# Optimization experiments

Hardware: AMD Instinct MI355X
Metric: run time of the kernel (lower is better)

The kernel has to match this reference:

```python
import jax, jax.numpy as jnp
import numpy as np

BATCH, SEQ, D_DIM, H = 8, 4096, 256, 64


def _log_step_init(u, dmin=0.001, dmax=0.1):
    lg_dmin, lg_dmax = np.log(dmin), np.log(dmax)
    return u * (lg_dmax - lg_dmin) + lg_dmin


def _make_hippo_nplr(N):
    q = np.arange(N)
    hip = np.sqrt((2 * q[:, None] + 1) * (2 * q[None, :] + 1))
    hip = np.where(q[:, None] > q[None, :], hip, 0.0) + np.diag(q + 1.0)
    hip = -hip
    p = np.sqrt(q + 0.5)
    S = hip + np.outer(p, p)  # NPLR: A = S - p p^T
    lam, V = np.linalg.eig(S)
    P = V.conj().T @ p
    B = V.conj().T @ (np.sqrt(2.0) * p)
    return lam.astype(np.complex64), P.astype(np.complex64), B.astype(np.complex64)


def _ri(z):
    return np.stack([z.real, z.imag], axis=-1).astype(np.float32)


def _cx(p):
    return p[..., 0] + 1j * p[..., 1]


def setup_inputs() -> dict:
    key = jax.random.key(0)
    k1, k2, k3 = jax.random.split(key, 3)
    lam, P, B = _make_hippo_nplr(H)
    lam_ri = jnp.asarray(_ri(lam))                      # (H, 2)
    P_ri = jnp.asarray(_ri(P))                          # (H, 2)
    B_ri = jnp.asarray(np.tile(_ri(B)[None], (D_DIM, 1, 1)))  # (D, H, 2)
    C_ri = jax.random.uniform(k1, (D_DIM, H, 2), dtype=jnp.float32)  # torch.rand complex
    Dp = jnp.ones((1, 1, D_DIM), dtype=jnp.float32)
    log_delta = jnp.asarray(
        _log_step_init(np.asarray(jax.random.uniform(k2, (D_DIM,), dtype=jnp.float32)))
    ).astype(jnp.float32)
    x = jax.random.normal(k3, (BATCH, SEQ, D_DIM), dtype=jnp.float32)
    return {"x": x, "lam_ri": lam_ri, "P_ri": P_ri, "B_ri": B_ri,
            "C_ri": C_ri, "D": Dp, "log_delta": log_delta}


def reference(x, lam_ri, P_ri, B_ri, C_ri, D, log_delta):
    # S4 DPLR generating-function kernel via Woodbury / Cauchy dot-products + iFFT conv.
    lam, P, B, C = _cx(lam_ri), _cx(P_ri), _cx(B_ri), _cx(C_ri)  # (H,), (H,), (D,H), (D,H)
    delta = jnp.exp(log_delta)                                   # (D,)
    L = x.shape[1]
    z = jnp.exp(2j * jnp.pi * jnp.arange(L) / L).astype(jnp.complex64)  # roots of unity (L,)
    coef = 2.0 / (1.0 + z)                                        # (L,)
    g = (2.0 * (1.0 - z) / (1.0 + z))[None, :] / delta[:, None].astype(jnp.complex64)  # (D, L)
    cauchy = 1.0 / (g[:, :, None] - lam[None, None, :])           # (D, L, H) -- R(z) diagonal
    # Woodbury: C (R - R P P* R / (1 + P* R P)) B  as 4 Cauchy dot products
    k00 = jnp.einsum("dh,dlh->dl", C * B, cauchy)
    k01 = jnp.einsum("dh,dlh->dl", C * P[None, :], cauchy)
    k10 = jnp.einsum("dh,dlh->dl", P.conj()[None, :] * B, cauchy)
    k11 = jnp.einsum("h,dlh->dl", P.conj() * P, cauchy)
    at_roots = coef[None, :] * (k00 - k01 * k10 / (1.0 + k11))    # (D, L)
    K = jnp.fft.ifft(at_roots, axis=-1).real.astype(x.dtype)      # (D, L) time-domain kernel
    # circular convolution along the sequence axis, per channel
    Xf = jnp.fft.fft(x, axis=1)                                   # (B, L, D)
    Kf = jnp.fft.fft(K, axis=-1)                                  # (D, L)
    y = jnp.fft.ifft(Xf * Kf.T[None, :, :], axis=1).real.astype(x.dtype)
    return y + D * x
```

## Files before the change

kernel.cpp:

```cpp
#include <hip/hip_runtime.h>
#include <math.h>

#ifndef M_PI
#define M_PI 3.14159265358979323846
#endif

#define BB 8
#define LL 4096
#define DD 256
#define HH 64

__device__ __forceinline__ float2 cmulf(float2 a, float2 b) {
    return make_float2(a.x*b.x - a.y*b.y, a.x*b.y + a.y*b.x);
}
__device__ __forceinline__ float2 cmul_cs(float2 a, float c, float s) {
    return make_float2(a.x*c - a.y*s, a.x*s + a.y*c);
}
__device__ __forceinline__ float2 cadd(float2 a, float2 b){return make_float2(a.x+b.x, a.y+b.y);}
__device__ __forceinline__ float2 csub(float2 a, float2 b){return make_float2(a.x-b.x, a.y-b.y);}

#define DR4(i) ((((i)&3)<<2)|((i)>>2))
#define SPW(k) ((((k)>>4)*17) + ((k)&15))

template<int SGN>
__device__ __forceinline__ void r4(float2& a, float2& b, float2& c, float2& d) {
    float2 e0 = cadd(a, c), e1 = csub(a, c);
    float2 o0 = cadd(b, d), o1 = csub(b, d);
    float2 j1 = (SGN < 0) ? make_float2(o1.y, -o1.x) : make_float2(-o1.y, o1.x);
    a = cadd(e0, o0);
    b = cadd(e1, j1);
    c = csub(e0, o0);
    d = csub(e1, j1);
}

template<int SGN>
__device__ __forceinline__ void fft16(float2 v[16]) {
    const float C16[10] = {1.f, 0.92387953f, 0.70710678f, 0.38268343f, 0.f,
                           -0.38268343f, -0.70710678f, -0.92387953f, -1.f, -0.92387953f};
    const float S16[10] = {0.f, 0.38268343f, 0.70710678f, 0.92387953f, 1.f,
                           0.92387953f, 0.70710678f, 0.38268343f, 0.f, -0.38268343f};
#pragma unroll
    for (int a0 = 0; a0 < 4; ++a0)
        r4<SGN>(v[a0], v[a0+4], v[a0+8], v[a0+12]);
#pragma unroll
    for (int a0 = 1; a0 < 4; ++a0) {
#pragma unroll
        for (int j0 = 1; j0 < 4; ++j0) {
            const int e = a0*j0;
            const float cc = C16[e];
            const float ss = (SGN < 0) ? -S16[e] : S16[e];
            v[a0 + 4*j0] = cmul_cs(v[a0 + 4*j0], cc, ss);
        }
    }
#pragma unroll
    for (int j0 = 0; j0 < 4; ++j0)
        r4<SGN>(v[4*j0+0], v[4*j0+1], v[4*j0+2], v[4*j0+3]);
}

__device__ __forceinline__ float2 woodbury_coef(
    float k00r, float k00i, float k01r, float k01i,
    float k10r, float k10i, float k11r, float k11i, float tc)
{
    float wr = 1.f + k11r, wi = k11i;
    float winv = __builtin_amdgcn_rcpf(wr*wr + wi*wi);
    float qr = k01r*k10r - k01i*k10i;
    float qi = k01r*k10i + k01i*k10r;
    float dr = (qr*wr + qi*wi) * winv;
    float di = (qi*wr - qr*wi) * winv;
    float rr = k00r - dr, ri = k00i - di;
    return make_float2(rr - tc*ri, tc*rr + ri);
}

__global__ __launch_bounds__(256)
void s4_cauchy_kf(const float* __restrict__ lam_ri,
                  const float* __restrict__ P_ri,
                  const float* __restrict__ B_ri,
                  const float* __restrict__ C_ri,
                  const float* __restrict__ Dp,
                  const float* __restrict__ log_delta,
                  float2* __restrict__ Kf)
{
    __shared__ float4 WA[HH];
    __shared__ float4 WB[HH];
    __shared__ float  WC[HH];
    const int d   = blockIdx.y;
    const int tid = threadIdx.x;
    if (tid < HH) {
        const int h = tid;
        float br = B_ri[(d*HH + h)*2 + 0], bi = B_ri[(d*HH + h)*2 + 1];
        float cr = C_ri[(d*HH + h)*2 + 0], ci = C_ri[(d*HH + h)*2 + 1];
        float pr = P_ri[h*2 + 0], pi = P_ri[h*2 + 1];
        WA[h] = make_float4(cr*br - ci*bi, cr*bi + ci*br,
                            cr*pr - ci*pi, cr*pi + ci*pr);
        WB[h] = make_float4(pr*br + pi*bi, pr*bi - pi*br,
                            pr*pr + pi*pi, -lam_ri[h*2+0]);
        WC[h] = lam_ri[h*2+1];
    }
    __syncthreads();
    const int l = blockIdx.x * blockDim.x + tid;
    if (l > 2048) return;
    const float delta = expf(log_delta[d]);
    const float dterm = Dp[d];
    const float SCALE = 0.5f / 4096.f;

    if (l == 2048) {
        float sr = 0.f;
        for (int h = 0; h < HH; ++h) sr += WA[h].x;
        Kf[(size_t)d*LL + 2048] = make_float2((0.5f*delta*sr + dterm)*SCALE, 0.f);
        return;
    }

    float sn, cs;
    sincosf((float)l * (float)(M_PI/4096.0), &sn, &cs);
    const float t = sn * __builtin_amdgcn_rcpf(cs);
    const float G = -2.f * t * __builtin_amdgcn_rcpf(delta);

    float a00r=0,a00i=0,a01r=0,a01i=0,a10r=0,a10i=0,a11r=0,a11i=0;
    float b00r=0,b00i=0,b01r=0,b01i=0,b10r=0,b10i=0,b11r=0,b11i=0;

#pragma unroll 4
    for (int h = 0; h < HH; ++h) {
        const float4 wa = WA[h];
        const float4 wb = WB[h];
        const float  lih = WC[h];
        const float  nr  = wb.w;
        const float  nr2 = nr*nr;
        {
            const float ni  = G - lih;
            const float inv = __builtin_amdgcn_rcpf(nr2 + ni*ni);
            const float rr  = nr*inv, ri = -ni*inv;
            a00r += wa.x*rr - wa.y*ri;  a00i += wa.x*ri + wa.y*rr;
            a01r += wa.z*rr - wa.w*ri;  a01i += wa.z*ri + wa.w*rr;
            a10r += wb.x*rr - wb.y*ri;  a10i += wb.x*ri + wb.y*rr;
            a11r += wb.z*rr;            a11i += wb.z*ri;
        }
        {
            const float ni  = -G - lih;
            const float inv = __builtin_amdgcn_rcpf(nr2 + ni*ni);
            const float rr  = nr*inv, ri = -ni*inv;
            b00r += wa.x*rr - wa.y*ri;  b00i += wa.x*ri + wa.y*rr;
            b01r += wa.z*rr - wa.w*ri;  b01i += wa.z*ri + wa.w*rr;
            b10r += wb.x*rr - wb.y*ri;  b10i += wb.x*ri + wb.y*rr;
            b11r += wb.z*rr;            b11i += wb.z*ri;
        }
    }

    float2 ar1 = woodbury_coef(a00r,a00i,a01r,a01i,a10r,a10i,a11r,a11i, -t);
    float2 ar2 = woodbury_coef(b00r,b00i,b01r,b01i,b10r,b10i,b11r,b11i, +t);

    float2 kf = make_float2((0.5f*(ar1.x + ar2.x) + dterm)*SCALE,
                            (0.5f*(ar1.y - ar2.y))*SCALE);
    Kf[(size_t)d*LL + l] = kf;
}

__global__ __launch_bounds__(256)
void s4_fftconv(const float* __restrict__ x, const float2* __restrict__ Kf,
                float* __restrict__ y)
{
    __shared__ float2 As[4352];
    const int tid = threadIdx.x;
    const int p  = ((blockIdx.x & 7) << 7) | (blockIdx.x >> 3);
    const int b  = p >> 7;
    const int d2 = p & 127;

    const float2* xp = (const float2*)x + ((size_t)b*LL)*(DD/2) + d2;
    float2*       yp = (float2*)y       + ((size_t)b*LL)*(DD/2) + d2;

    float2 v[16];

    {
        const int r = tid;
#pragma unroll
        for (int a = 0; a < 16; ++a)
            v[a] = xp[(size_t)(a*256 + r)*(DD/2)];
        fft16<-1>(v);
        float2 base; sincosf(-(float)(2.0*M_PI/4096.0)*(float)r, &base.y, &base.x);
        float2 w = make_float2(1.f, 0.f);
#pragma unroll
        for (int k0 = 0; k0 < 16; ++k0) {
            As[17*r + k0] = cmulf(v[DR4(k0)], w);
            w = cmulf(w, base);
        }
    }
    __syncthreads();

    {
        const int k0 = tid >> 4, c = tid & 15;
#pragma unroll
        for (int bb = 0; bb < 16; ++bb)
            v[bb] = As[272*bb + 17*c + k0];
        __syncthreads();
        fft16<-1>(v);
        float2 base; sincosf(-(float)(2.0*M_PI/256.0)*(float)c, &base.y, &base.x);
        float2 w = make_float2(1.f, 0.f);
#pragma unroll
        for (int m0 = 0; m0 < 16; ++m0) {
            As[272*k0 + 17*c + m0] = cmulf(v[DR4(m0)], w);
            w = cmulf(w, base);
        }
    }
    __syncthreads();

    {
        const int k0 = tid >> 4, m0 = tid & 15;
#pragma unroll
        for (int c = 0; c < 16; ++c)
            v[c] = As[272*k0 + 17*c + m0];
        __syncthreads();
        fft16<-1>(v);
        const int s17 = 17*m0 + k0;
#pragma unroll
        for (int m1 = 0; m1 < 16; ++m1)
            As[s17 + 272*m1] = v[DR4(m1)];
    }
    __syncthreads();

    {
        const float2* Keb = Kf + (size_t)(2*d2)  *LL;
        const float2* Kob = Kf + (size_t)(2*d2+1)*LL;
#pragma unroll
        for (int i = 0; i < 9; ++i) {
            int k = tid + (i << 8);
            if (k <= 2048) {
                int mk = (4096 - k) & 4095;
                float2 Zk = As[SPW(k)];
                float2 Zm = As[SPW(mk)];
                float2 Ke = Keb[k];
                float2 Ko = Kob[k];
                float2 S  = make_float2(Ke.x + Ko.x, Ke.y + Ko.y);
                float2 Df = make_float2(Ke.x - Ko.x, Ke.y - Ko.y);
                float2 cZm = make_float2(Zm.x, -Zm.y);
                float2 t0 = cmulf(Zk,  S);
                float2 t1 = cmulf(cZm, Df);
                float2 t2 = cmulf(cZm, S);
                float2 t3 = cmulf(Zk,  Df);
                As[SPW(k)]  = make_float2(t0.x + t1.x,   t0.y + t1.y);
                As[SPW(mk)] = make_float2(t2.x + t3.x, -(t2.y + t3.y));
            }
        }
    }
    __syncthreads();

    {
        const int k0 = tid >> 4, m0 = tid & 15;
        const int s17 = 17*m0 + k0;
#pragma unroll
        for (int m1 = 0; m1 < 16; ++m1)
            v[m1] = As[s17 + 272*m1];
        __syncthreads();
        fft16<1>(v);
        float2 base; sincosf((float)(2.0*M_PI/256.0)*(float)m0, &base.y, &base.x);
        float2 w = make_float2(1.f, 0.f);
#pragma unroll
        for (int c = 0; c < 16; ++c) {
            As[272*k0 + 17*c + m0] = cmulf(v[DR4(c)], w);
            w = cmulf(w, base);
        }
    }
    __syncthreads();

    {
        const int k0 = tid >> 4, c = tid & 15;
#pragma unroll
        for (int m0 = 0; m0 < 16; ++m0)
            v[m0] = As[272*k0 + 17*c + m0];
        __syncthreads();
        fft16<1>(v);
        float2 w, st;
        sincosf((float)(2.0*M_PI/4096.0)*(float)(c*k0), &w.y, &w.x);
        sincosf((float)(2.0*M_PI/256.0)*(float)k0,      &st.y, &st.x);
#pragma unroll
        for (int bb = 0; bb < 16; ++bb) {
            As[272*bb + 17*c + k0] = cmulf(v[DR4(bb)], w);
            w = cmulf(w, st);
        }
    }
    __syncthreads();

    {
        const int r = tid;
#pragma unroll
        for (int k0 = 0; k0 < 16; ++k0)
            v[k0] = As[17*r + k0];
        fft16<1>(v);
#pragma unroll
        for (int a = 0; a < 16; ++a)
            yp[(size_t)(a*256 + r)*(DD/2)] = v[DR4(a)];
    }
}

extern "C" void kernel_launch(void* const* d_in, const int* in_sizes, int n_in,
                              void* d_out, int out_size, void* d_ws, size_t ws_size,
                              hipStream_t stream)
{
    (void)in_sizes; (void)n_in; (void)out_size; (void)ws_size;
    const float* x         = (const float*)d_in[0];
    const float* lam_ri    = (const float*)d_in[1];
    const float* P_ri      = (const float*)d_in[2];
    const float* B_ri      = (const float*)d_in[3];
    const float* C_ri      = (const float*)d_in[4];
    const float* Dp        = (const float*)d_in[5];
    const float* log_delta = (const float*)d_in[6];
    float* y = (float*)d_out;

    float2* Kf = (float2*)d_ws;

    s4_cauchy_kf<<<dim3(9, DD), 256, 0, stream>>>(lam_ri, P_ri, B_ri, C_ri, Dp, log_delta, Kf);
    s4_fftconv<<<dim3(BB*DD/2), 256, 0, stream>>>(x, Kf, y);
}
```

Measured before the change: 178.3 us.

## Share Cauchy reciprocals across conjugate pairs and prefetch kernel spectrum early

The Cauchy kernel now computes two frequencies per thread and handles both +G and -G with one shared reciprocal of the product of denominators. It also derives the k10/k11 sums of the mirrored term by conjugation, since P-only weights are real-symmetric. The grid shrinks from 9 to 4 blocks per channel. The FFT-conv kernel issues its loads of the Kf spectrum before the first FFT stage, so their latency overlaps the FFT. Costs are higher register pressure from 18 prefetched float2 values and slightly different rounding from the fused reciprocal.

```diff
diff --git a/kernel.cpp b/kernel.cpp
--- a/kernel.cpp
+++ b/kernel.cpp
@@ -97,60 +97,86 @@
         WC[h] = lam_ri[h*2+1];
     }
     __syncthreads();
-    const int l = blockIdx.x * blockDim.x + tid;
-    if (l > 2048) return;
+    const int t0 = blockIdx.x * blockDim.x + tid;
     const float delta = expf(log_delta[d]);
     const float dterm = Dp[d];
     const float SCALE = 0.5f / 4096.f;
 
-    if (l == 2048) {
-        float sr = 0.f;
-        for (int h = 0; h < HH; ++h) sr += WA[h].x;
-        Kf[(size_t)d*LL + 2048] = make_float2((0.5f*delta*sr + dterm)*SCALE, 0.f);
-        return;
-    }
-
-    float sn, cs;
-    sincosf((float)l * (float)(M_PI/4096.0), &sn, &cs);
-    const float t = sn * __builtin_amdgcn_rcpf(cs);
-    const float G = -2.f * t * __builtin_amdgcn_rcpf(delta);
-
-    float a00r=0,a00i=0,a01r=0,a01i=0,a10r=0,a10i=0,a11r=0,a11i=0;
-    float b00r=0,b00i=0,b01r=0,b01i=0,b10r=0,b10i=0,b11r=0,b11i=0;
+    const int l1 = t0;
+    const int l2 = t0 + 1024;
+
+    float sn1, cs1, sn2, cs2;
+    sincosf((float)l1 * (float)(M_PI/4096.0), &sn1, &cs1);
+    sincosf((float)l2 * (float)(M_PI/4096.0), &sn2, &cs2);
+    const float invd = __builtin_amdgcn_rcpf(delta);
+    const float tt1 = sn1 * __builtin_amdgcn_rcpf(cs1);
+    const float tt2 = sn2 * __builtin_amdgcn_rcpf(cs2);
+    const float G1 = -2.f * tt1 * invd;
+    const float G2 = -2.f * tt2 * invd;
+
+    float a00r1=0,a00i1=0,a01r1=0,a01i1=0,a10r1=0,a10i1=0,a11r1=0,a11i1=0;
+    float b00r1=0,b00i1=0,b01r1=0,b01i1=0;
+    float a00r2=0,a00i2=0,a01r2=0,a01i2=0,a10r2=0,a10i2=0,a11r2=0,a11i2=0;
+    float b00r2=0,b00i2=0,b01r2=0,b01i2=0;
+    float sr2048 = 0.f;
 
 #pragma unroll 4
     for (int h = 0; h < HH; ++h) {
         const float4 wa = WA[h];
         const float4 wb = WB[h];
-        const float  lih = WC[h];
+        const float  li = WC[h];
         const float  nr  = wb.w;
         const float  nr2 = nr*nr;
+        sr2048 += wa.x;
         {
-            const float ni  = G - lih;
-            const float inv = __builtin_amdgcn_rcpf(nr2 + ni*ni);
-            const float rr  = nr*inv, ri = -ni*inv;
-            a00r += wa.x*rr - wa.y*ri;  a00i += wa.x*ri + wa.y*rr;
-            a01r += wa.z*rr - wa.w*ri;  a01i += wa.z*ri + wa.w*rr;
-            a10r += wb.x*rr - wb.y*ri;  a10i += wb.x*ri + wb.y*rr;
-            a11r += wb.z*rr;            a11i += wb.z*ri;
+            const float nip = G1 - li, nim = G1 + li;
+            const float dp = fmaf(nip, nip, nr2);
+            const float dm = fmaf(nim, nim, nr2);
+            const float ip = __builtin_amdgcn_rcpf(dp*dm);
+            const float invp = dm*ip, invm = dp*ip;
+            const float rrp = nr*invp, rip = -nip*invp;
+            const float rrm = nr*invm, rim =  nim*invm;
+            a00r1 += wa.x*rrp - wa.y*rip;  a00i1 += wa.x*rip + wa.y*rrp;
+            a01r1 += wa.z*rrp - wa.w*rip;  a01i1 += wa.z*rip + wa.w*rrp;
+            a10r1 += wb.x*rrp - wb.y*rip;  a10i1 += wb.x*rip + wb.y*rrp;
+            a11r1 += wb.z*rrp;             a11i1 += wb.z*rip;
+            b00r1 += wa.x*rrm - wa.y*rim;  b00i1 += wa.x*rim + wa.y*rrm;
+            b01r1 += wa.z*rrm - wa.w*rim;  b01i1 += wa.z*rim + wa.w*rrm;
         }
         {
-            const float ni  = -G - lih;
-            const float inv = __builtin_amdgcn_rcpf(nr2 + ni*ni);
-            const float rr  = nr*inv, ri = -ni*inv;
-            b00r += wa.x*rr - wa.y*ri;  b00i += wa.x*ri + wa.y*rr;
-            b01r += wa.z*rr - wa.w*ri;  b01i += wa.z*ri + wa.w*rr;
-            b10r += wb.x*rr - wb.y*ri;  b10i += wb.x*ri + wb.y*rr;
-            b11r += wb.z*rr;            b11i += wb.z*ri;
-        }
-    }
-
-    float2 ar1 = woodbury_coef(a00r,a00i,a01r,a01i,a10r,a10i,a11r,a11i, -t);
-    float2 ar2 = woodbury_coef(b00r,b00i,b01r,b01i,b10r,b10i,b11r,b11i, +t);
-
-    float2 kf = make_float2((0.5f*(ar1.x + ar2.x) + dterm)*SCALE,
-                            (0.5f*(ar1.y - ar2.y))*SCALE);
-    Kf[(size_t)d*LL + l] = kf;
+            const float nip = G2 - li, nim = G2 + li;
+            const float dp = fmaf(nip, nip, nr2);
+            const float dm = fmaf(nim, nim, nr2);
+            const float ip = __builtin_amdgcn_rcpf(dp*dm);
+            const float invp = dm*ip, invm = dp*ip;
+            const float rrp = nr*invp, rip = -nip*invp;
+            const float rrm = nr*invm, rim =  nim*invm;
+            a00r2 += wa.x*rrp - wa.y*rip;  a00i2 += wa.x*rip + wa.y*rrp;
+            a01r2 += wa.z*rrp - wa.w*rip;  a01i2 += wa.z*rip + wa.w*rrp;
+            a10r2 += wb.x*rrp - wb.y*rip;  a10i2 += wb.x*rip + wb.y*rrp;
+            a11r2 += wb.z*rrp;             a11i2 += wb.z*rip;
+            b00r2 += wa.x*rrm - wa.y*rim;  b00i2 += wa.x*rim + wa.y*rrm;
+            b01r2 += wa.z*rrm - wa.w*rim;  b01i2 += wa.z*rim + wa.w*rrm;
+        }
+    }
+
+    {
+        float2 ar1 = woodbury_coef(a00r1,a00i1,a01r1,a01i1,a10r1,a10i1,a11r1,a11i1, -tt1);
+        float2 ar2 = woodbury_coef(b00r1,b00i1,b01r1,b01i1,a10r1,-a10i1,a11r1,-a11i1, +tt1);
+        float2 kf = make_float2((0.5f*(ar1.x + ar2.x) + dterm)*SCALE,
+                                (0.5f*(ar1.y - ar2.y))*SCALE);
+        Kf[(size_t)d*LL + l1] = kf;
+    }
+    {
+        float2 ar1 = woodbury_coef(a00r2,a00i2,a01r2,a01i2,a10r2,a10i2,a11r2,a11i2, -tt2);
+        float2 ar2 = woodbury_coef(b00r2,b00i2,b01r2,b01i2,a10r2,-a10i2,a11r2,-a11i2, +tt2);
+        float2 kf = make_float2((0.5f*(ar1.x + ar2.x) + dterm)*SCALE,
+                                (0.5f*(ar1.y - ar2.y))*SCALE);
+        Kf[(size_t)d*LL + l2] = kf;
+    }
+    if (t0 == 0) {
+        Kf[(size_t)d*LL + 2048] = make_float2((0.5f*delta*sr2048 + dterm)*SCALE, 0.f);
+    }
 }
 
 __global__ __launch_bounds__(256)
@@ -165,6 +191,8 @@
 
     const float2* xp = (const float2*)x + ((size_t)b*LL)*(DD/2) + d2;
     float2*       yp = (float2*)y       + ((size_t)b*LL)*(DD/2) + d2;
+    const float2* Keb = Kf + (size_t)(2*d2)  *LL;
+    const float2* Kob = Kf + (size_t)(2*d2+1)*LL;
 
     float2 v[16];
 
@@ -173,6 +201,17 @@
 #pragma unroll
         for (int a = 0; a < 16; ++a)
             v[a] = xp[(size_t)(a*256 + r)*(DD/2)];
+    }
+    float2 pKe[9], pKo[9];
+#pragma unroll
+    for (int i = 0; i < 9; ++i) {
+        int k = tid + (i << 8); if (k > 2048) k = 2048;
+        pKe[i] = Keb[k];
+        pKo[i] = Kob[k];
+    }
+
+    {
+        const int r = tid;
         fft16<-1>(v);
         float2 base; sincosf(-(float)(2.0*M_PI/4096.0)*(float)r, &base.y, &base.x);
         float2 w = make_float2(1.f, 0.f);
@@ -216,8 +255,6 @@
     __syncthreads();
 
     {
-        const float2* Keb = Kf + (size_t)(2*d2)  *LL;
-        const float2* Kob = Kf + (size_t)(2*d2+1)*LL;
 #pragma unroll
         for (int i = 0; i < 9; ++i) {
             int k = tid + (i << 8);
@@ -225,8 +262,8 @@
                 int mk = (4096 - k) & 4095;
                 float2 Zk = As[SPW(k)];
                 float2 Zm = As[SPW(mk)];
-                float2 Ke = Keb[k];
-                float2 Ko = Kob[k];
+                float2 Ke = pKe[i];
+                float2 Ko = pKo[i];
                 float2 S  = make_float2(Ke.x + Ko.x, Ke.y + Ko.y);
                 float2 Df = make_float2(Ke.x - Ko.x, Ke.y - Ko.y);
                 float2 cZm = make_float2(Zm.x, -Zm.y);
@@ -305,6 +342,6 @@
 
     float2* Kf = (float2*)d_ws;
 
-    s4_cauchy_kf<<<dim3(9, DD), 256, 0, stream>>>(lam_ri, P_ri, B_ri, C_ri, Dp, log_delta, Kf);
+    s4_cauchy_kf<<<dim3(4, DD), 256, 0, stream>>>(lam_ri, P_ri, B_ri, C_ri, Dp, log_delta, Kf);
     s4_fftconv<<<dim3(BB*DD/2), 256, 0, stream>>>(x, Kf, y);
 }
```

After: 163.9 us. -8.1%, faster.
